# Kernel optimization log

Measured on AMD Instinct MI355X. Metric: run time of the kernel, lower is better.

The kernel has to match this reference:

```python
import math
import jax, jax.numpy as jnp
import numpy as np

THETA = 10000.0

def _rotate_half(x):
    # lucidrains interleaved pairs: (d r) with r=2
    x = x.reshape(*x.shape[:-1], -1, 2)
    x1, x2 = x[..., 0], x[..., 1]
    return jnp.stack([-x2, x1], axis=-1).reshape(*x.shape[:-2], -1)

def _apply_rotary(x):
    # x: [B, H, S, D]
    seq_len, d = x.shape[-2], x.shape[-1]
    inv_freq = 1.0 / (THETA ** (jnp.arange(0, d, 2, dtype=jnp.float32) / d))  # [D/2]
    t = jnp.arange(seq_len, dtype=jnp.float32)
    freqs = t[:, None] * inv_freq[None, :]                 # [S, D/2]
    freqs = jnp.repeat(freqs, 2, axis=-1)                  # [S, D] interleaved
    cos, sin = jnp.cos(freqs), jnp.sin(freqs)
    return x * cos + _rotate_half(x) * sin

def setup_inputs() -> dict:
    key = jax.random.key(0)
    k1, k2, k3, k4 = jax.random.split(key, 4)
    B, H, S, D = 2, 16, 2048, 64
    q = jax.random.normal(k1, (B, H, S, D), dtype=jnp.float32)
    k = jax.random.normal(k2, (B, H, S, D), dtype=jnp.float32)
    v = jax.random.normal(k3, (B, H, S, D), dtype=jnp.float32)
    mask = jax.random.randint(k4, (B, 1, S, S), 0, 2, dtype=jnp.int32)
    return {"q": q, "k": k, "v": v, "mask": mask}

def reference(q, k, v, mask):
    d = k.shape[-1]
    qr = _apply_rotary(q)
    kr = _apply_rotary(k)
    score = jnp.einsum('bhqd,bhkd->bhqk', qr, kr) / math.sqrt(d)
    score = jnp.where(mask == 0, jnp.float32(-10000.0), score)
    score = jax.nn.softmax(score, axis=-1)
    out = jnp.einsum('bhqk,bhkd->bhqd', score, v)
    return (out, score)
```

## Files before the change

### kernel.cpp

```cpp
#include <hip/hip_runtime.h>
#include <hip/hip_fp16.h>

#define NB 2
#define NH 16
#define NS 2048
#define ND 64

typedef __attribute__((ext_vector_type(8))) _Float16 half8;
typedef __attribute__((ext_vector_type(4))) _Float16 half4;
typedef __attribute__((ext_vector_type(4))) float float4v;

static constexpr int NE = NB * NH * NS * ND;
static constexpr int TPB = 512;

__device__ __forceinline__ void wg_barrier_lds() {
    asm volatile("s_waitcnt lgkmcnt(0)" ::: "memory");
    __builtin_amdgcn_s_barrier();
    __builtin_amdgcn_sched_barrier(0);
}

static constexpr int ROPE_BLKS = (NE / 2) / 256;
static constexpr int VT_BLKS   = NE / 256;
static constexpr int MP_BLKS   = (NB * NS * NS) / 256;

__global__ void prep_kernel(const float* __restrict__ q,
                            const float* __restrict__ k,
                            const float* __restrict__ v,
                            const int* __restrict__ mask,
                            _Float16* __restrict__ qr,
                            _Float16* __restrict__ kr6,
                            _Float16* __restrict__ v4,
                            unsigned int* __restrict__ mp) {
    int blk = blockIdx.x;
    if (blk < ROPE_BLKS) {
        int idx = blk * 256 + threadIdx.x;
        int i   = idx & 31;
        int row = idx >> 5;
        int s   = row & (NS - 1);
        int bh  = row >> 11;

        float inv_freq = expf((float)i * -0.2878231366242710f);
        float ang = (float)s * inv_freq;
        float sn, cs;
        sincosf(ang, &sn, &cs);

        size_t base = (size_t)row * ND + 2 * i;
        float q0 = q[base], q1 = q[base + 1];
        float k0 = k[base], k1 = k[base + 1];
        qr[base]     = (_Float16)(q0 * cs - q1 * sn);
        qr[base + 1] = (_Float16)(q1 * cs + q0 * sn);

        int oct = i >> 2;
        int j0  = (2 * i) & 7;
        size_t t6 = ((size_t)(bh * 128 + (s >> 4)) * 8 + oct) * 128 + (s & 15) * 8 + j0;
        kr6[t6]     = (_Float16)(k0 * cs - k1 * sn);
        kr6[t6 + 1] = (_Float16)(k1 * cs + k0 * sn);
    } else if (blk < ROPE_BLKS + VT_BLKS) {
        int idx = (blk - ROPE_BLKS) * 256 + threadIdx.x;
        int j    = idx & 3;
        int lm   = (idx >> 2) & 15;
        int kq   = (idx >> 6) & 3;
        int dblk = (idx >> 8) & 3;
        int kt   = (idx >> 10) & 127;
        int bh   = idx >> 17;
        int key  = kt * 16 + kq * 4 + j;
        int d    = dblk * 16 + lm;
        v4[idx] = (_Float16)v[((size_t)bh * NS + key) * ND + d];
    } else {
        size_t idx = (size_t)(blk - ROPE_BLKS - VT_BLKS) * 256 + threadIdx.x;
        unsigned long long bal = __ballot(mask[idx] != 0);
        int l = threadIdx.x & 63;
        if (l == 0)       mp[idx >> 5] = (unsigned int)bal;
        else if (l == 32) mp[idx >> 5] = (unsigned int)(bal >> 32);
    }
}

static constexpr int TPH    = 264;
static constexpr int WSLICE = 16 * TPH;

__global__ __launch_bounds__(TPB, 4)
void attn_reg_kernel(const _Float16* __restrict__ qr,
                     const _Float16* __restrict__ kr6,
                     const _Float16* __restrict__ v4,
                     const unsigned int* __restrict__ mp,
                     float* __restrict__ out,
                     float* __restrict__ score) {
    __shared__ unsigned int maskb[16 * 64];
    __shared__ float        sums8[8][16];
    __shared__ _Float16     pool[8 * WSLICE];

    int wgid = (blockIdx.x & 7) * 512 + (blockIdx.x >> 3);
    int qt = wgid & 127;
    int bh = wgid >> 7;
    int b  = bh >> 4;
    int q0 = qt * 16;

    int tid = threadIdx.x;
    int w   = tid >> 6;
    int l   = tid & 63;
    int lm  = l & 15;
    int lp  = l >> 4;

    {
        const unsigned int* mrow = mp + ((size_t)b * NS + q0) * 64;
        for (int i = tid; i < 16 * 64; i += TPB) maskb[i] = mrow[i];
    }

    const _Float16* qrow = qr + ((size_t)bh * NS + q0 + lm) * ND;
    half8 a0 = *(const half8*)(qrow + lp * 8);
    half8 a1 = *(const half8*)(qrow + 32 + lp * 8);
    const _Float16* k6 = kr6 + (size_t)bh * 128 * 1024;
    _Float16* tw = pool + w * WSLICE;
    wg_barrier_lds();

    float4v ac0 = {0.f, 0.f, 0.f, 0.f};
    float4v ac1 = {0.f, 0.f, 0.f, 0.f};
    float4v ac2 = {0.f, 0.f, 0.f, 0.f};
    float4v ac3 = {0.f, 0.f, 0.f, 0.f};
    const _Float16* vb = v4 + (size_t)bh * 128 * 1024 + l * 4;
    float ps = 0.0f;
#pragma unroll
    for (int t = 0; t < 16; ++t) {
        int kt = w * 16 + t;
        const _Float16* kp = k6 + (size_t)kt * 1024 + l * 8;
        half8 b0 = *(const half8*)(kp);
        half8 b1 = *(const half8*)(kp + 512);
        float4v acc = {0.f, 0.f, 0.f, 0.f};
        acc = __builtin_amdgcn_mfma_f32_16x16x32_f16(b0, a0, acc, 0, 0, 0);
        acc = __builtin_amdgcn_mfma_f32_16x16x32_f16(b1, a1, acc, 0, 0, 0);
        int keyb = kt * 16 + lp * 4;
        unsigned int mw = maskb[lm * 64 + (keyb >> 5)];
        int bit0 = keyb & 31;
        half4 ep;
#pragma unroll
        for (int r = 0; r < 4; ++r) {
            float ev = ((mw >> (bit0 + r)) & 1u) ? __expf(acc[r] * 0.125f) : 0.0f;
            ps += ev;
            ep[r] = (_Float16)ev;
        }
        *(half4*)(tw + lm * TPH + t * 16 + lp * 4) = ep;

        const _Float16* vp = vb + (size_t)kt * 1024;
        half4 af0 = *(const half4*)(vp);
        half4 af1 = *(const half4*)(vp + 256);
        half4 af2 = *(const half4*)(vp + 512);
        half4 af3 = *(const half4*)(vp + 768);
        __builtin_amdgcn_s_setprio(1);
        ac0 = __builtin_amdgcn_mfma_f32_16x16x16f16(af0, ep, ac0, 0, 0, 0);
        ac1 = __builtin_amdgcn_mfma_f32_16x16x16f16(af1, ep, ac1, 0, 0, 0);
        ac2 = __builtin_amdgcn_mfma_f32_16x16x16f16(af2, ep, ac2, 0, 0, 0);
        ac3 = __builtin_amdgcn_mfma_f32_16x16x16f16(af3, ep, ac3, 0, 0, 0);
        __builtin_amdgcn_s_setprio(0);
    }
    ps += __shfl_xor(ps, 16);
    ps += __shfl_xor(ps, 32);
    if (lp == 0) sums8[w][lm] = ps;
    wg_barrier_lds();

    {
        float s = 0.0f;
#pragma unroll
        for (int ww = 0; ww < 8; ++ww) s += sums8[ww][lm];
        float iv = (s > 0.0f) ? (1.0f / s) : 0.0f;
        float* sbase = score + ((size_t)bh * NS + q0) * NS + w * 256;
#pragma unroll
        for (int r = 0; r < 16; ++r) {
            float ivr = __shfl(iv, r);
            half4 hv = *(const half4*)(tw + r * TPH + l * 4);
            float4v f;
            f[0] = (float)hv[0] * ivr;
            f[1] = (float)hv[1] * ivr;
            f[2] = (float)hv[2] * ivr;
            f[3] = (float)hv[3] * ivr;
            __builtin_nontemporal_store(f, (float4v*)(sbase + (size_t)r * NS + l * 4));
        }
    }
    asm volatile("s_waitcnt lgkmcnt(0)" ::: "memory");
    __builtin_amdgcn_sched_barrier(0);

    {
        float* ow = (float*)tw + lm * 64 + lp * 4;
#pragma unroll
        for (int r = 0; r < 4; ++r) {
            ow[ 0 + r] = ac0[r];
            ow[16 + r] = ac1[r];
            ow[32 + r] = ac2[r];
            ow[48 + r] = ac3[r];
        }
    }
    wg_barrier_lds();

    {
        float* orow = out + ((size_t)bh * NS + q0) * ND;
        for (int i = tid; i < 16 * 64; i += TPB) {
            int r = i >> 6;
            float s = 0.0f;
#pragma unroll
            for (int ww = 0; ww < 8; ++ww) s += sums8[ww][r];
            float iv = (s > 0.0f) ? (1.0f / s) : 0.0f;
            float acc = 0.0f;
#pragma unroll
            for (int ww = 0; ww < 8; ++ww)
                acc += ((const float*)(pool + ww * WSLICE))[i];
            __builtin_nontemporal_store(acc * iv, &orow[i]);
        }
    }
}

extern "C" void kernel_launch(void* const* d_in, const int* in_sizes, int n_in,
                              void* d_out, int out_size, void* d_ws, size_t ws_size,
                              hipStream_t stream) {
    const float* q    = (const float*)d_in[0];
    const float* k    = (const float*)d_in[1];
    const float* v    = (const float*)d_in[2];
    const int*   mask = (const int*)d_in[3];

    float* out   = (float*)d_out;
    float* score = out + (size_t)NE;

    _Float16* qrw = (_Float16*)d_ws;
    _Float16* kr6 = qrw + NE;
    _Float16* v4w = kr6 + NE;
    unsigned int* mp = (unsigned int*)(v4w + NE);

    prep_kernel<<<dim3(ROPE_BLKS + VT_BLKS + MP_BLKS), dim3(256), 0, stream>>>(
        q, k, v, mask, qrw, kr6, v4w, mp);
    attn_reg_kernel<<<dim3(NB * NH * (NS / 16)), dim3(TPB), 0, stream>>>(
        qrw, kr6, v4w, mp, out, score);
}
```

Measured before the change: 171.3 us.

## Process two 16-row query tiles per workgroup to reuse K and V loads

Each workgroup now handles 32 query rows instead of 16, computing two score tiles against the same K and V fragments and holding the second tile's probabilities in registers until the first tile's scores are written out. This halves global K/V traffic per query row and halves the grid size. In exchange it roughly doubles accumulator and probability register use, which may lower occupancy under the launch bounds, and serializes the score write-out through the shared LDS slice.

```diff
diff --git a/kernel.cpp b/kernel.cpp
--- a/kernel.cpp
+++ b/kernel.cpp
@@ -10,12 +10,16 @@
 typedef __attribute__((ext_vector_type(4))) _Float16 half4;
 typedef __attribute__((ext_vector_type(4))) float float4v;
 
-static constexpr int NE = NB * NH * NS * ND;
+static constexpr int NE  = NB * NH * NS * ND;
 static constexpr int TPB = 512;
 
 __device__ __forceinline__ void wg_barrier_lds() {
     asm volatile("s_waitcnt lgkmcnt(0)" ::: "memory");
     __builtin_amdgcn_s_barrier();
+    __builtin_amdgcn_sched_barrier(0);
+}
+__device__ __forceinline__ void wave_lds_guard() {
+    asm volatile("s_waitcnt lgkmcnt(0)" ::: "memory");
     __builtin_amdgcn_sched_barrier(0);
 }
 
@@ -85,15 +89,16 @@
                      const unsigned int* __restrict__ mp,
                      float* __restrict__ out,
                      float* __restrict__ score) {
-    __shared__ unsigned int maskb[16 * 64];
-    __shared__ float        sums8[8][16];
+    __shared__ unsigned int maskb[32 * 64];
+    __shared__ float        sumsA[8][16];
+    __shared__ float        sumsB[8][16];
     __shared__ _Float16     pool[8 * WSLICE];
 
-    int wgid = (blockIdx.x & 7) * 512 + (blockIdx.x >> 3);
-    int qt = wgid & 127;
-    int bh = wgid >> 7;
+    int wgid = (blockIdx.x & 7) * 256 + (blockIdx.x >> 3);
+    int qt = wgid & 63;
+    int bh = wgid >> 6;
     int b  = bh >> 4;
-    int q0 = qt * 16;
+    int q0 = qt * 32;
 
     int tid = threadIdx.x;
     int w   = tid >> 6;
@@ -103,64 +108,81 @@
 
     {
         const unsigned int* mrow = mp + ((size_t)b * NS + q0) * 64;
-        for (int i = tid; i < 16 * 64; i += TPB) maskb[i] = mrow[i];
-    }
-
-    const _Float16* qrow = qr + ((size_t)bh * NS + q0 + lm) * ND;
-    half8 a0 = *(const half8*)(qrow + lp * 8);
-    half8 a1 = *(const half8*)(qrow + 32 + lp * 8);
+        for (int i = tid; i < 32 * 64; i += TPB) maskb[i] = mrow[i];
+    }
+
+    const _Float16* qrowA = qr + ((size_t)bh * NS + q0 + lm) * ND;
+    const _Float16* qrowB = qrowA + 16 * ND;
+    half8 a0A = *(const half8*)(qrowA + lp * 8);
+    half8 a1A = *(const half8*)(qrowA + 32 + lp * 8);
+    half8 a0B = *(const half8*)(qrowB + lp * 8);
+    half8 a1B = *(const half8*)(qrowB + 32 + lp * 8);
     const _Float16* k6 = kr6 + (size_t)bh * 128 * 1024;
+    const _Float16* vb = v4 + (size_t)bh * 128 * 1024 + l * 4;
     _Float16* tw = pool + w * WSLICE;
     wg_barrier_lds();
 
-    float4v ac0 = {0.f, 0.f, 0.f, 0.f};
-    float4v ac1 = {0.f, 0.f, 0.f, 0.f};
-    float4v ac2 = {0.f, 0.f, 0.f, 0.f};
-    float4v ac3 = {0.f, 0.f, 0.f, 0.f};
-    const _Float16* vb = v4 + (size_t)bh * 128 * 1024 + l * 4;
-    float ps = 0.0f;
+    float4v acA0 = {0.f, 0.f, 0.f, 0.f}, acA1 = {0.f, 0.f, 0.f, 0.f};
+    float4v acA2 = {0.f, 0.f, 0.f, 0.f}, acA3 = {0.f, 0.f, 0.f, 0.f};
+    float4v acB0 = {0.f, 0.f, 0.f, 0.f}, acB1 = {0.f, 0.f, 0.f, 0.f};
+    float4v acB2 = {0.f, 0.f, 0.f, 0.f}, acB3 = {0.f, 0.f, 0.f, 0.f};
+    half4 earrB[16];
+    float psA = 0.0f, psB = 0.0f;
 #pragma unroll
     for (int t = 0; t < 16; ++t) {
         int kt = w * 16 + t;
         const _Float16* kp = k6 + (size_t)kt * 1024 + l * 8;
         half8 b0 = *(const half8*)(kp);
         half8 b1 = *(const half8*)(kp + 512);
-        float4v acc = {0.f, 0.f, 0.f, 0.f};
-        acc = __builtin_amdgcn_mfma_f32_16x16x32_f16(b0, a0, acc, 0, 0, 0);
-        acc = __builtin_amdgcn_mfma_f32_16x16x32_f16(b1, a1, acc, 0, 0, 0);
+        float4v sa = {0.f, 0.f, 0.f, 0.f};
+        float4v sb = {0.f, 0.f, 0.f, 0.f};
+        sa = __builtin_amdgcn_mfma_f32_16x16x32_f16(b0, a0A, sa, 0, 0, 0);
+        sa = __builtin_amdgcn_mfma_f32_16x16x32_f16(b1, a1A, sa, 0, 0, 0);
+        sb = __builtin_amdgcn_mfma_f32_16x16x32_f16(b0, a0B, sb, 0, 0, 0);
+        sb = __builtin_amdgcn_mfma_f32_16x16x32_f16(b1, a1B, sb, 0, 0, 0);
         int keyb = kt * 16 + lp * 4;
-        unsigned int mw = maskb[lm * 64 + (keyb >> 5)];
+        int word = keyb >> 5;
         int bit0 = keyb & 31;
-        half4 ep;
+        unsigned int mwA = maskb[lm * 64 + word];
+        unsigned int mwB = maskb[(lm + 16) * 64 + word];
+        half4 epA, epB;
 #pragma unroll
         for (int r = 0; r < 4; ++r) {
-            float ev = ((mw >> (bit0 + r)) & 1u) ? __expf(acc[r] * 0.125f) : 0.0f;
-            ps += ev;
-            ep[r] = (_Float16)ev;
-        }
-        *(half4*)(tw + lm * TPH + t * 16 + lp * 4) = ep;
-
+            float evA = ((mwA >> (bit0 + r)) & 1u) ? __expf(sa[r] * 0.125f) : 0.0f;
+            float evB = ((mwB >> (bit0 + r)) & 1u) ? __expf(sb[r] * 0.125f) : 0.0f;
+            psA += evA; psB += evB;
+            epA[r] = (_Float16)evA;
+            epB[r] = (_Float16)evB;
+        }
+        *(half4*)(tw + lm * TPH + t * 16 + lp * 4) = epA;
+        earrB[t] = epB;
         const _Float16* vp = vb + (size_t)kt * 1024;
         half4 af0 = *(const half4*)(vp);
         half4 af1 = *(const half4*)(vp + 256);
         half4 af2 = *(const half4*)(vp + 512);
         half4 af3 = *(const half4*)(vp + 768);
         __builtin_amdgcn_s_setprio(1);
-        ac0 = __builtin_amdgcn_mfma_f32_16x16x16f16(af0, ep, ac0, 0, 0, 0);
-        ac1 = __builtin_amdgcn_mfma_f32_16x16x16f16(af1, ep, ac1, 0, 0, 0);
-        ac2 = __builtin_amdgcn_mfma_f32_16x16x16f16(af2, ep, ac2, 0, 0, 0);
-        ac3 = __builtin_amdgcn_mfma_f32_16x16x16f16(af3, ep, ac3, 0, 0, 0);
+        acA0 = __builtin_amdgcn_mfma_f32_16x16x16f16(af0, epA, acA0, 0, 0, 0);
+        acA1 = __builtin_amdgcn_mfma_f32_16x16x16f16(af1, epA, acA1, 0, 0, 0);
+        acA2 = __builtin_amdgcn_mfma_f32_16x16x16f16(af2, epA, acA2, 0, 0, 0);
+        acA3 = __builtin_amdgcn_mfma_f32_16x16x16f16(af3, epA, acA3, 0, 0, 0);
+        acB0 = __builtin_amdgcn_mfma_f32_16x16x16f16(af0, epB, acB0, 0, 0, 0);
+        acB1 = __builtin_amdgcn_mfma_f32_16x16x16f16(af1, epB, acB1, 0, 0, 0);
+        acB2 = __builtin_amdgcn_mfma_f32_16x16x16f16(af2, epB, acB2, 0, 0, 0);
+        acB3 = __builtin_amdgcn_mfma_f32_16x16x16f16(af3, epB, acB3, 0, 0, 0);
         __builtin_amdgcn_s_setprio(0);
     }
-    ps += __shfl_xor(ps, 16);
-    ps += __shfl_xor(ps, 32);
-    if (lp == 0) sums8[w][lm] = ps;
+    psA += __shfl_xor(psA, 16);
+    psA += __shfl_xor(psA, 32);
+    psB += __shfl_xor(psB, 16);
+    psB += __shfl_xor(psB, 32);
+    if (lp == 0) { sumsA[w][lm] = psA; sumsB[w][lm] = psB; }
     wg_barrier_lds();
 
     {
         float s = 0.0f;
 #pragma unroll
-        for (int ww = 0; ww < 8; ++ww) s += sums8[ww][lm];
+        for (int ww = 0; ww < 8; ++ww) s += sumsA[ww][lm];
         float iv = (s > 0.0f) ? (1.0f / s) : 0.0f;
         float* sbase = score + ((size_t)bh * NS + q0) * NS + w * 256;
 #pragma unroll
@@ -175,28 +197,56 @@
             __builtin_nontemporal_store(f, (float4v*)(sbase + (size_t)r * NS + l * 4));
         }
     }
-    asm volatile("s_waitcnt lgkmcnt(0)" ::: "memory");
-    __builtin_amdgcn_sched_barrier(0);
-
-    {
-        float* ow = (float*)tw + lm * 64 + lp * 4;
+    wave_lds_guard();
+#pragma unroll
+    for (int t = 0; t < 16; ++t)
+        *(half4*)(tw + lm * TPH + t * 16 + lp * 4) = earrB[t];
+    wave_lds_guard();
+
+    {
+        float s = 0.0f;
+#pragma unroll
+        for (int ww = 0; ww < 8; ++ww) s += sumsB[ww][lm];
+        float iv = (s > 0.0f) ? (1.0f / s) : 0.0f;
+        float* sbase = score + ((size_t)bh * NS + q0 + 16) * NS + w * 256;
+#pragma unroll
+        for (int r = 0; r < 16; ++r) {
+            float ivr = __shfl(iv, r);
+            half4 hv = *(const half4*)(tw + r * TPH + l * 4);
+            float4v f;
+            f[0] = (float)hv[0] * ivr;
+            f[1] = (float)hv[1] * ivr;
+            f[2] = (float)hv[2] * ivr;
+            f[3] = (float)hv[3] * ivr;
+            __builtin_nontemporal_store(f, (float4v*)(sbase + (size_t)r * NS + l * 4));
+        }
+    }
+    wave_lds_guard();
+    {
+        float* owA = (float*)tw + lm * 64 + lp * 4;
+        float* owB = owA + 1024;
 #pragma unroll
         for (int r = 0; r < 4; ++r) {
-            ow[ 0 + r] = ac0[r];
-            ow[16 + r] = ac1[r];
-            ow[32 + r] = ac2[r];
-            ow[48 + r] = ac3[r];
+            owA[ 0 + r] = acA0[r]; owA[16 + r] = acA1[r];
+            owA[32 + r] = acA2[r]; owA[48 + r] = acA3[r];
+            owB[ 0 + r] = acB0[r]; owB[16 + r] = acB1[r];
+            owB[32 + r] = acB2[r]; owB[48 + r] = acB3[r];
         }
     }
     wg_barrier_lds();
 
     {
         float* orow = out + ((size_t)bh * NS + q0) * ND;
-        for (int i = tid; i < 16 * 64; i += TPB) {
+        for (int i = tid; i < 32 * 64; i += TPB) {
             int r = i >> 6;
             float s = 0.0f;
-#pragma unroll
-            for (int ww = 0; ww < 8; ++ww) s += sums8[ww][r];
+            if (r < 16) {
+#pragma unroll
+                for (int ww = 0; ww < 8; ++ww) s += sumsA[ww][r];
+            } else {
+#pragma unroll
+                for (int ww = 0; ww < 8; ++ww) s += sumsB[ww][r - 16];
+            }
             float iv = (s > 0.0f) ? (1.0f / s) : 0.0f;
             float acc = 0.0f;
 #pragma unroll
@@ -225,6 +275,6 @@
 
     prep_kernel<<<dim3(ROPE_BLKS + VT_BLKS + MP_BLKS), dim3(256), 0, stream>>>(
         q, k, v, mask, qrw, kr6, v4w, mp);
-    attn_reg_kernel<<<dim3(NB * NH * (NS / 16)), dim3(TPB), 0, stream>>>(
+    attn_reg_kernel<<<dim3(NB * NH * (NS / 32)), dim3(TPB), 0, stream>>>(
         qrw, kr6, v4w, mp, out, score);
 }
```

After: 196.7 us. 1.15x slower.
